# Kernel tuning notes

Measured on AMD Instinct MI355X. Metric: run time of the kernel, lower is better.

## Reference

```python
import jax, jax.numpy as jnp
import numpy as np

B, T, H = 32, 4096, 256

def setup_inputs() -> dict:
    key = jax.random.key(0)
    k1, k2, k3, k4, k5 = jax.random.split(key, 5)
    hidden = jax.random.normal(k1, (B, H), dtype=jnp.float32)
    encoder_outputs = jax.random.normal(k2, (T, B, H), dtype=jnp.float32)
    # nn.Linear(2H, H): weight [H, 2H], bias [H] (kaiming-uniform-ish scale)
    bound = 1.0 / np.sqrt(2 * H)
    attn_w = jax.random.uniform(k3, (H, 2 * H), minval=-bound, maxval=bound, dtype=jnp.float32)
    attn_b = jax.random.uniform(k4, (H,), minval=-bound, maxval=bound, dtype=jnp.float32)
    v = jax.random.uniform(k5, (H,), dtype=jnp.float32)  # torch.rand -> U[0,1)
    return {"hidden": hidden, "encoder_outputs": encoder_outputs,
            "attn_w": attn_w, "attn_b": attn_b, "v": v}

def reference(hidden, encoder_outputs, attn_w, attn_b, v):
    # hidden: [B, H]; encoder_outputs: [T, B, H]
    t = encoder_outputs.shape[0]
    enc = jnp.transpose(encoder_outputs, (1, 0, 2))            # [B, T, H]
    h = jnp.broadcast_to(hidden[:, None, :], enc.shape)        # [B, T, H]
    temp = jnp.concatenate([h, enc], axis=2)                   # [B, T, 2H]
    energy = jax.nn.relu(jnp.einsum('btk,hk->bth', temp, attn_w) + attn_b)  # [B, T, H]
    scores = jnp.einsum('bth,h->bt', energy, v)                # [B, T]
    return jax.nn.softmax(scores, axis=1)[:, None, :]          # [B, 1, T]
```

## Files before the change

### kernel.cpp

```cpp
#include <hip/hip_runtime.h>
#include <hip/hip_bf16.h>

#define B_SZ 32
#define T_SZ 4096
#define H_SZ 256
#define BH   8192
#define SROW 72

typedef __attribute__((ext_vector_type(8))) short bf16x8;
typedef __attribute__((ext_vector_type(4))) float f32x4;

static __device__ __forceinline__ short f2bf(float x) {
    unsigned u = __float_as_uint(x);
    u += 0x7fffu + ((u >> 16) & 1u);
    return (short)(u >> 16);
}

static __device__ __forceinline__ bf16x8 cvt8(f32x4 a, f32x4 b) {
    bf16x8 r;
    r[0] = f2bf(a[0]); r[1] = f2bf(a[1]); r[2] = f2bf(a[2]); r[3] = f2bf(a[3]);
    r[4] = f2bf(b[0]); r[5] = f2bf(b[1]); r[6] = f2bf(b[2]); r[7] = f2bf(b[3]);
    return r;
}

__global__ __launch_bounds__(256) void prep_kernel(
    const float* __restrict__ hidden, const float* __restrict__ attn_w,
    const float* __restrict__ attn_b, float* __restrict__ hp,
    short* __restrict__ wbf)
{
    const int h   = blockIdx.x;
    const int tid = threadIdx.x;
    __shared__ float wsh[H_SZ];

    wsh[tid] = attn_w[(size_t)h * 512 + tid];
    wbf[(size_t)h * H_SZ + tid] = f2bf(attn_w[(size_t)h * 512 + 256 + tid]);
    __syncthreads();

    const int b  = tid >> 3;
    const int kg = tid & 7;
    const float* hrow = hidden + b * H_SZ + kg * 32;
    const float* wrow = wsh + kg * 32;
    float s = 0.f;
#pragma unroll
    for (int j = 0; j < 32; j += 4) {
        f32x4 hv = *(const f32x4*)(hrow + j);
        s = fmaf(hv[0], wrow[j + 0], s);
        s = fmaf(hv[1], wrow[j + 1], s);
        s = fmaf(hv[2], wrow[j + 2], s);
        s = fmaf(hv[3], wrow[j + 3], s);
    }
#pragma unroll
    for (int off = 1; off < 8; off <<= 1) s += __shfl_xor(s, off, 8);
    if (kg == 0) hp[b * H_SZ + h] = s + attn_b[h];
}

__global__ __launch_bounds__(256, 3) void attn_main(
    const float* __restrict__ enc,
    const short* __restrict__ wbf,
    const float* __restrict__ hp,
    const float* __restrict__ v,
    float* __restrict__ scores)
{
    __shared__ __align__(16) short As[2][64 * SROW];
    __shared__ float part[4][64];

    const int blk  = blockIdx.x;
    const int b    = blk >> 6;
    const int t0   = (blk & 63) << 6;
    const int tid  = threadIdx.x;
    const int w    = tid >> 6;
    const int lane = tid & 63;
    const int r    = lane & 15;
    const int quad = lane >> 4;
    const int hbase = w * 64;

    const int srow = tid >> 2, sq = tid & 3;
    const float* sp = enc + (size_t)b * H_SZ + (size_t)(t0 + srow) * BH + sq * 16;
    short* sd0 = &As[0][0] + srow * SROW + sq * 16;
    short* sd1 = &As[1][0] + srow * SROW + sq * 16;

    const short* wp0 = wbf + (size_t)(hbase + 0 * 16 + r) * H_SZ + quad * 8;
    const short* wp1 = wbf + (size_t)(hbase + 1 * 16 + r) * H_SZ + quad * 8;
    const short* wp2 = wbf + (size_t)(hbase + 2 * 16 + r) * H_SZ + quad * 8;
    const short* wp3 = wbf + (size_t)(hbase + 3 * 16 + r) * H_SZ + quad * 8;

    f32x4 acc[4][4];
#pragma unroll
    for (int mt = 0; mt < 4; ++mt)
#pragma unroll
        for (int nt = 0; nt < 4; ++nt)
            acc[mt][nt] = (f32x4){0.f, 0.f, 0.f, 0.f};

    bf16x8 bc[2][4];
#pragma unroll
    for (int s = 0; s < 2; ++s) {
        bc[s][0] = *(const bf16x8*)(wp0 + s * 32);
        bc[s][1] = *(const bf16x8*)(wp1 + s * 32);
        bc[s][2] = *(const bf16x8*)(wp2 + s * 32);
        bc[s][3] = *(const bf16x8*)(wp3 + s * 32);
    }
    {
        f32x4 st[4];
#pragma unroll
        for (int j = 0; j < 4; ++j) st[j] = *(const f32x4*)(sp + 4 * j);
        ((bf16x8*)sd0)[0] = cvt8(st[0], st[1]);
        ((bf16x8*)sd0)[1] = cvt8(st[2], st[3]);
    }
    __syncthreads();

#pragma unroll
    for (int kc = 0; kc < 4; ++kc) {
        f32x4 stn[4];
        if (kc < 3) {
#pragma unroll
            for (int j = 0; j < 4; ++j)
                stn[j] = *(const f32x4*)(sp + (kc + 1) * 64 + 4 * j);
        }

        const short* abase = &As[kc & 1][0] + quad * 8;
#pragma unroll
        for (int s = 0; s < 2; ++s) {
            bf16x8 af[4];
#pragma unroll
            for (int mt = 0; mt < 4; ++mt)
                af[mt] = *(const bf16x8*)(abase + (mt * 16 + r) * SROW + s * 32);
#pragma unroll
            for (int mt = 0; mt < 4; ++mt)
#pragma unroll
                for (int nt = 0; nt < 4; ++nt)
                    acc[mt][nt] = __builtin_amdgcn_mfma_f32_16x16x32_bf16(
                        af[mt], bc[s][nt], acc[mt][nt], 0, 0, 0);
        }

        if (kc < 3) {
            const int ko = (kc + 1) * 64;
#pragma unroll
            for (int s = 0; s < 2; ++s) {
                bc[s][0] = *(const bf16x8*)(wp0 + ko + s * 32);
                bc[s][1] = *(const bf16x8*)(wp1 + ko + s * 32);
                bc[s][2] = *(const bf16x8*)(wp2 + ko + s * 32);
                bc[s][3] = *(const bf16x8*)(wp3 + ko + s * 32);
            }
            short* d = ((kc + 1) & 1) ? sd1 : sd0;
            ((bf16x8*)d)[0] = cvt8(stn[0], stn[1]);
            ((bf16x8*)d)[1] = cvt8(stn[2], stn[3]);
            __syncthreads();
        }
    }

    float hpv[4], vv[4];
#pragma unroll
    for (int nt = 0; nt < 4; ++nt) {
        const int h = hbase + nt * 16 + r;
        hpv[nt] = hp[b * H_SZ + h];
        vv[nt]  = v[h];
    }

#pragma unroll
    for (int mt = 0; mt < 4; ++mt) {
#pragma unroll
        for (int reg = 0; reg < 4; ++reg) {
            float s = 0.f;
#pragma unroll
            for (int nt = 0; nt < 4; ++nt) {
                float e = hpv[nt] + acc[mt][nt][reg];
                e = fmaxf(e, 0.f);
                s = fmaf(vv[nt], e, s);
            }
#pragma unroll
            for (int off = 1; off < 16; off <<= 1) s += __shfl_xor(s, off, 16);
            if (r == 0) part[w][mt * 16 + quad * 4 + reg] = s;
        }
    }
    __syncthreads();
    if (tid < 64) {
        float sc = part[0][tid] + part[1][tid] + part[2][tid] + part[3][tid];
        scores[b * T_SZ + t0 + tid] = sc;
    }
}

__global__ __launch_bounds__(1024) void softmax_kernel(
    const float* __restrict__ scores, float* __restrict__ out)
{
    const int b   = blockIdx.x;
    const int tid = threadIdx.x;
    const float* s = scores + b * T_SZ;
    float*       o = out    + b * T_SZ;

    float loc[4];
    float m = -3.0e38f;
#pragma unroll
    for (int i = 0; i < 4; ++i) {
        loc[i] = s[tid + i * 1024];
        m = fmaxf(m, loc[i]);
    }
    __shared__ float redm[16], reds[16];
#pragma unroll
    for (int off = 32; off > 0; off >>= 1) m = fmaxf(m, __shfl_xor(m, off, 64));
    if ((tid & 63) == 0) redm[tid >> 6] = m;
    __syncthreads();
#pragma unroll
    for (int i = 0; i < 16; ++i) m = fmaxf(m, redm[i]);

    float sum = 0.f;
#pragma unroll
    for (int i = 0; i < 4; ++i) {
        loc[i] = __expf(loc[i] - m);
        sum += loc[i];
    }
#pragma unroll
    for (int off = 32; off > 0; off >>= 1) sum += __shfl_xor(sum, off, 64);
    if ((tid & 63) == 0) reds[tid >> 6] = sum;
    __syncthreads();
    sum = 0.f;
#pragma unroll
    for (int i = 0; i < 16; ++i) sum += reds[i];
    const float inv = 1.0f / sum;
#pragma unroll
    for (int i = 0; i < 4; ++i) o[tid + i * 1024] = loc[i] * inv;
}

extern "C" void kernel_launch(void* const* d_in, const int* in_sizes, int n_in,
                              void* d_out, int out_size, void* d_ws, size_t ws_size,
                              hipStream_t stream) {
    const float* hidden = (const float*)d_in[0];
    const float* enc    = (const float*)d_in[1];
    const float* attn_w = (const float*)d_in[2];
    const float* attn_b = (const float*)d_in[3];
    const float* v      = (const float*)d_in[4];
    float* out = (float*)d_out;

    float* hp     = (float*)d_ws;
    float* scores = hp + B_SZ * H_SZ;
    short* wbf    = (short*)(scores + B_SZ * T_SZ);

    hipLaunchKernelGGL(prep_kernel, dim3(H_SZ), dim3(256), 0, stream,
                       hidden, attn_w, attn_b, hp, wbf);
    hipLaunchKernelGGL(attn_main, dim3(B_SZ * (T_SZ / 64)), dim3(256), 0, stream,
                       enc, wbf, hp, v, scores);
    hipLaunchKernelGGL(softmax_kernel, dim3(B_SZ), dim3(1024), 0, stream,
                       scores, out);
}
```

Measured before the change: 225.4 us.

## Tile encoder rows contiguously in native T-major order with transposed hidden projection

The main kernel now takes 64 consecutive rows of encoder_outputs in its native [T,B,H] memory order instead of 64 time steps of a single batch. Each tile therefore reads one contiguous 64 KB region rather than 64 strided 1 KB rows, which is meant to improve DRAM and TLB locality. Because a tile now spans two time steps across all 32 batches, the hidden projection is stored transposed so each lane can load per-batch bias values as vectors. Scores are scattered back into [B,T] order at the end, which makes the 64-float score stores non-contiguous.

Measured after the change: 226.4 us. Within noise of the previous version (+0.5%).

```diff
diff --git a/kernel.cpp b/kernel.cpp
--- a/kernel.cpp
+++ b/kernel.cpp
@@ -4,7 +4,7 @@
 #define B_SZ 32
 #define T_SZ 4096
 #define H_SZ 256
-#define BH   8192
+#define M_SZ (T_SZ * B_SZ)
 #define SROW 72
 
 typedef __attribute__((ext_vector_type(8))) short bf16x8;
@@ -25,7 +25,7 @@
 
 __global__ __launch_bounds__(256) void prep_kernel(
     const float* __restrict__ hidden, const float* __restrict__ attn_w,
-    const float* __restrict__ attn_b, float* __restrict__ hp,
+    const float* __restrict__ attn_b, float* __restrict__ hpT,
     short* __restrict__ wbf)
 {
     const int h   = blockIdx.x;
@@ -51,13 +51,13 @@
     }
 #pragma unroll
     for (int off = 1; off < 8; off <<= 1) s += __shfl_xor(s, off, 8);
-    if (kg == 0) hp[b * H_SZ + h] = s + attn_b[h];
+    if (kg == 0) hpT[h * B_SZ + b] = s + attn_b[h];
 }
 
 __global__ __launch_bounds__(256, 3) void attn_main(
     const float* __restrict__ enc,
     const short* __restrict__ wbf,
-    const float* __restrict__ hp,
+    const float* __restrict__ hpT,
     const float* __restrict__ v,
     float* __restrict__ scores)
 {
@@ -65,8 +65,7 @@
     __shared__ float part[4][64];
 
     const int blk  = blockIdx.x;
-    const int b    = blk >> 6;
-    const int t0   = (blk & 63) << 6;
+    const int m0   = blk << 6;
     const int tid  = threadIdx.x;
     const int w    = tid >> 6;
     const int lane = tid & 63;
@@ -75,7 +74,7 @@
     const int hbase = w * 64;
 
     const int srow = tid >> 2, sq = tid & 3;
-    const float* sp = enc + (size_t)b * H_SZ + (size_t)(t0 + srow) * BH + sq * 16;
+    const float* sp = enc + (size_t)(m0 + srow) * H_SZ + sq * 16;
     short* sd0 = &As[0][0] + srow * SROW + sq * 16;
     short* sd1 = &As[1][0] + srow * SROW + sq * 16;
 
@@ -148,12 +147,14 @@
         }
     }
 
-    float hpv[4], vv[4];
+    float vv[4];
+    f32x4 hpv[2][4];
 #pragma unroll
     for (int nt = 0; nt < 4; ++nt) {
         const int h = hbase + nt * 16 + r;
-        hpv[nt] = hp[b * H_SZ + h];
-        vv[nt]  = v[h];
+        vv[nt] = v[h];
+        hpv[0][nt] = *(const f32x4*)(hpT + h * B_SZ + quad * 4);
+        hpv[1][nt] = *(const f32x4*)(hpT + h * B_SZ + 16 + quad * 4);
     }
 
 #pragma unroll
@@ -163,7 +164,7 @@
             float s = 0.f;
 #pragma unroll
             for (int nt = 0; nt < 4; ++nt) {
-                float e = hpv[nt] + acc[mt][nt][reg];
+                float e = hpv[mt & 1][nt][reg] + acc[mt][nt][reg];
                 e = fmaxf(e, 0.f);
                 s = fmaf(vv[nt], e, s);
             }
@@ -175,7 +176,9 @@
     __syncthreads();
     if (tid < 64) {
         float sc = part[0][tid] + part[1][tid] + part[2][tid] + part[3][tid];
-        scores[b * T_SZ + t0 + tid] = sc;
+        const int b = tid & 31;
+        const int t = (m0 + tid) >> 5;
+        scores[b * T_SZ + t] = sc;
     }
 }
 
@@ -230,14 +233,14 @@
     const float* v      = (const float*)d_in[4];
     float* out = (float*)d_out;
 
-    float* hp     = (float*)d_ws;
-    float* scores = hp + B_SZ * H_SZ;
+    float* hpT    = (float*)d_ws;
+    float* scores = hpT + H_SZ * B_SZ;
     short* wbf    = (short*)(scores + B_SZ * T_SZ);
 
     hipLaunchKernelGGL(prep_kernel, dim3(H_SZ), dim3(256), 0, stream,
-                       hidden, attn_w, attn_b, hp, wbf);
-    hipLaunchKernelGGL(attn_main, dim3(B_SZ * (T_SZ / 64)), dim3(256), 0, stream,
-                       enc, wbf, hp, v, scores);
+                       hidden, attn_w, attn_b, hpT, wbf);
+    hipLaunchKernelGGL(attn_main, dim3(M_SZ / 64), dim3(256), 0, stream,
+                       enc, wbf, hpT, v, scores);
     hipLaunchKernelGGL(softmax_kernel, dim3(B_SZ), dim3(1024), 0, stream,
                        scores, out);
 }
```
